# Kernel optimization log

Measured on AMD Instinct MI355X. Metric: run time of the kernel, lower is better.

## Reference

```python
import jax, jax.numpy as jnp
import numpy as np

N = 25000      # nodes
E = 400000     # edges (before self-loops)
F_IN = 128     # num_node_features
HID = 16       # hidden_channels
HEADS = 12     # GAT heads
OUT = 32       # output_channels


def setup_inputs() -> dict:
    key = jax.random.key(0)
    ks = jax.random.split(key, 16)
    def glorot(k, shape):
        fan_in = shape[0]
        return jax.random.normal(k, shape, jnp.float32) / np.sqrt(fan_in)
    return {
        "x": jax.random.normal(ks[0], (N, 1, F_IN), jnp.float32),
        "edge_index": jax.random.randint(ks[1], (2, E), 0, N, jnp.int64),
        # GCNConv 1
        "W1": glorot(ks[2], (F_IN, HID)),
        "b1": jnp.zeros((HID,), jnp.float32),
        # GATConv (heads=12, concat)
        "Wg": glorot(ks[3], (HID, HEADS * HID)),
        "att_src": jax.random.normal(ks[4], (HEADS, HID), jnp.float32) * 0.1,
        "att_dst": jax.random.normal(ks[5], (HEADS, HID), jnp.float32) * 0.1,
        "bg": jnp.zeros((HEADS * HID,), jnp.float32),
        # GCNConv 2 and 3
        "W2": glorot(ks[6], (HEADS * HID, HID)),
        "b2": jnp.zeros((HID,), jnp.float32),
        "W3": glorot(ks[7], (HID, HID)),
        "b3": jnp.zeros((HID,), jnp.float32),
        # final Linear
        "Wlin": glorot(ks[8], (HID, OUT)),
        "blin": jnp.zeros((OUT,), jnp.float32),
    }


def _add_self_loops(edge_index, n):
    loop = jnp.arange(n, dtype=edge_index.dtype)
    src = jnp.concatenate([edge_index[0], loop])
    dst = jnp.concatenate([edge_index[1], loop])
    return src, dst


def _gcn_conv(x, W, b, src, dst, n):
    # PyG GCNConv: symmetric normalization with self-loops (already in src/dst)
    h = x @ W                                            # [N, C]
    deg = jax.ops.segment_sum(jnp.ones_like(dst, jnp.float32), dst, n)
    dinv = jnp.where(deg > 0, jax.lax.rsqrt(deg), 0.0)   # deg^-0.5
    norm = dinv[src] * dinv[dst]                         # [E']
    out = jax.ops.segment_sum(h[src] * norm[:, None], dst, n)
    return out + b


def _gat_conv(x, Wg, att_src, att_dst, bg, src, dst, n):
    # PyG GATConv, concat=True, negative_slope=0.2, self-loops in src/dst
    h = (x @ Wg).reshape(n, HEADS, HID)                  # [N, H, C]
    a_s = jnp.sum(h * att_src, axis=-1)                  # [N, H]
    a_d = jnp.sum(h * att_dst, axis=-1)                  # [N, H]
    e = a_s[src] + a_d[dst]                              # [E', H]
    e = jnp.where(e > 0, e, 0.2 * e)                     # leaky_relu
    m = jax.ops.segment_max(e, dst, n)                   # stable softmax per dst
    ex = jnp.exp(e - m[dst])
    denom = jax.ops.segment_sum(ex, dst, n)
    alpha = ex / denom[dst]                              # [E', H]
    out = jax.ops.segment_sum(alpha[:, :, None] * h[src], dst, n)  # [N, H, C]
    return out.reshape(n, HEADS * HID) + bg


def reference(x, edge_index, W1, b1, Wg, att_src, att_dst, bg, W2, b2, W3, b3, Wlin, blin):
    n = x.shape[0]
    src, dst = _add_self_loops(edge_index, n)
    xs = x.squeeze(1)                                    # [N, F]
    x1 = jax.nn.relu(_gcn_conv(xs, W1, b1, src, dst, n))
    # dropout p=0.5 is identity in eval mode
    x2 = jax.nn.elu(_gat_conv(x1, Wg, att_src, att_dst, bg, src, dst, n))
    x3 = jax.nn.relu(_gcn_conv(x2, W2, b2, src, dst, n))
    x4 = jax.nn.relu(_gcn_conv(x3, W3, b3, src, dst, n)) + x3
    x4 = jnp.mean(x4, axis=0, keepdims=True)             # [1, HID]
    return x4 @ Wlin + blin                              # [1, OUT]
```

## Files before the change

kernel.cpp:

```cpp
#include <hip/hip_runtime.h>

#define F_IN 128
#define HID 16
#define HEADS 12
#define HF (HEADS*HID)
#define OUT_C 32

__global__ void k_detect(const int* __restrict__ ei, int E, int* __restrict__ flag) {
    int t = threadIdx.x;
    long long half = (long long)E;
    int acc = 0;
    #pragma unroll
    for (int i = 0; i < 8; i++) {
        long long k = ((long long)(t + i * 256) * half) / 2048;
        acc |= ei[2 * k + 1];
    }
    if (acc) atomicOr(&flag[1], 1);
}

__global__ void k_convert(const void* __restrict__ ei, int E, const int* __restrict__ flag,
                          int* __restrict__ src32, int* __restrict__ dst32,
                          int* __restrict__ count) {
    int e = blockIdx.x * blockDim.x + threadIdx.x;
    if (e >= E) return;
    int s, d;
    if (flag[1] == 0) {
        const long long* p = (const long long*)ei;
        s = (int)p[e];
        d = (int)p[(size_t)E + e];
    } else {
        const int* p = (const int*)ei;
        s = p[e];
        d = p[(size_t)E + e];
    }
    src32[e] = s;
    dst32[e] = d;
    atomicAdd(&count[d], 1);
}


__global__ void k_scan(const int* __restrict__ count, int* __restrict__ rowstart,
                       float* __restrict__ dinv, int n) {
    __shared__ int part[1024];
    int t = threadIdx.x;
    int chunk = (n + 1023) >> 10;
    int beg = t * chunk;
    int end = beg + chunk; if (end > n) end = n;
    int s = 0;
    for (int i = beg; i < end; i++) s += count[i];
    part[t] = s;
    __syncthreads();
    for (int off = 1; off < 1024; off <<= 1) {
        int v = (t >= off) ? part[t - off] : 0;
        __syncthreads();
        part[t] += v;
        __syncthreads();
    }
    int run = (t == 0) ? 0 : part[t - 1];
    for (int i = beg; i < end; i++) {
        rowstart[i] = run;
        int c = count[i];
        run += c;
        dinv[i] = rsqrtf((float)(c + 1));
    }
    if (t == 1023) rowstart[n] = run;
}

__global__ void k_fill(const int* __restrict__ srcA, const int* __restrict__ dstA, int E,
                       const int* __restrict__ rowstart, int* __restrict__ cursor,
                       int* __restrict__ csr) {
    int e = blockIdx.x * blockDim.x + threadIdx.x;
    if (e < E) {
        int d = dstA[e];
        int p = atomicAdd(&cursor[d], 1);
        csr[rowstart[d] + p] = srcA[e];
    }
}


__global__ void k_gemm1(const float* __restrict__ x, const float* __restrict__ W,
                        float* __restrict__ h, int n) {
    __shared__ float sW[F_IN * HID];
    __shared__ float sX[16][F_IN + 1];
    int t = threadIdx.x;
    for (int i = t; i < F_IN * HID; i += 256) sW[i] = W[i];
    int node0 = blockIdx.x * 16;
    for (int i = t; i < 16 * F_IN; i += 256) {
        int r = i >> 7, c = i & 127;
        int node = node0 + r;
        sX[r][c] = (node < n) ? x[node * F_IN + c] : 0.f;
    }
    __syncthreads();
    int ln = t >> 4, c = t & 15;
    float acc = 0.f;
    #pragma unroll 8
    for (int k = 0; k < F_IN; k++) acc += sX[ln][k] * sW[k * HID + c];
    int node = node0 + ln;
    if (node < n) h[node * HID + c] = acc;
}

__global__ void k_gemm_gat(const float* __restrict__ x1, const float* __restrict__ Wg,
                           const float* __restrict__ att_s, const float* __restrict__ att_d,
                           float* __restrict__ hg, float* __restrict__ a_s,
                           float* __restrict__ a_d, int n) {
    int c = threadIdx.x;
    int lane = c & 63;
    int hh = c >> 4, ci = c & 15;
    float ats = att_s[c];
    float atd = att_d[c];
    float wcol[HID];
    #pragma unroll
    for (int k = 0; k < HID; k++) wcol[k] = Wg[k * HF + c];
    for (int node = blockIdx.x; node < n; node += gridDim.x) {
        float xv = x1[node * HID + (lane & 15)];
        float acc = 0.f;
        #pragma unroll
        for (int k = 0; k < HID; k++) acc += __shfl(xv, k) * wcol[k];
        hg[(size_t)node * HF + c] = acc;
        float vs = acc * ats, vd = acc * atd;
        #pragma unroll
        for (int msk = 8; msk >= 1; msk >>= 1) {
            vs += __shfl_xor(vs, msk);
            vd += __shfl_xor(vd, msk);
        }
        if (ci == 0) {
            a_s[node * HEADS + hh] = vs;
            a_d[node * HEADS + hh] = vd;
        }
    }
}

__global__ void k_gemm2(const float* __restrict__ x2, const float* __restrict__ W,
                        float* __restrict__ h, int n) {
    __shared__ float sW[HF * HID];
    __shared__ float sX[16][HF + 1];
    int t = threadIdx.x;
    for (int i = t; i < HF * HID; i += 256) sW[i] = W[i];
    int node0 = blockIdx.x * 16;
    for (int i = t; i < 16 * HF; i += 256) {
        int r = i / HF, c = i % HF;
        int node = node0 + r;
        sX[r][c] = (node < n) ? x2[(size_t)node * HF + c] : 0.f;
    }
    __syncthreads();
    int ln = t >> 4, c = t & 15;
    float acc = 0.f;
    #pragma unroll 8
    for (int k = 0; k < HF; k++) acc += sX[ln][k] * sW[k * HID + c];
    int node = node0 + ln;
    if (node < n) h[node * HID + c] = acc;
}

__global__ void k_gemm3(const float* __restrict__ x3, const float* __restrict__ W,
                        float* __restrict__ h, int n) {
    __shared__ float sW[HID * HID];
    __shared__ float sX[16][HID + 1];
    int t = threadIdx.x;
    sW[t] = W[t];
    int node0 = blockIdx.x * 16;
    int r = t >> 4, cc = t & 15;
    int nd = node0 + r;
    sX[r][cc] = (nd < n) ? x3[nd * HID + cc] : 0.f;
    __syncthreads();
    float acc = 0.f;
    #pragma unroll
    for (int k = 0; k < HID; k++) acc += sX[r][k] * sW[k * HID + cc];
    if (nd < n) h[nd * HID + cc] = acc;
}


__global__ void k_gcn_agg(const float* __restrict__ h, const int* __restrict__ rowstart,
                          const int* __restrict__ csr, const float* __restrict__ dinv,
                          const float* __restrict__ bias, const float* __restrict__ resid,
                          float* __restrict__ out, int n) {
    int node = (blockIdx.x * blockDim.x + threadIdx.x) >> 6;
    int lane = threadIdx.x & 63;
    if (node >= n) return;
    int c = lane & 15, jj = lane >> 4;
    float dn = dinv[node];
    int base = rowstart[node], deg = rowstart[node + 1] - base;
    float acc = (jj == 0) ? h[node * HID + c] * dn : 0.f;
    for (int j = jj; j < deg; j += 4) {
        int s = csr[base + j];
        acc += h[s * HID + c] * dinv[s];
    }
    acc += __shfl_xor(acc, 16);
    acc += __shfl_xor(acc, 32);
    if (lane < 16) {
        float v = fmaxf(acc * dn + bias[c], 0.f);
        if (resid) v += resid[node * HID + c];
        out[node * HID + c] = v;
    }
}

__global__ void k_gat_agg(const float* __restrict__ hg, const float* __restrict__ a_s,
                          const float* __restrict__ a_d, const int* __restrict__ rowstart,
                          const int* __restrict__ csr, const float* __restrict__ bg,
                          float* __restrict__ x2, int n) {
    int node = (blockIdx.x * blockDim.x + threadIdx.x) >> 6;
    int lane = threadIdx.x & 63;
    if (node >= n) return;
    int base = rowstart[node], deg = rowstart[node + 1] - base;

    float mh[3], sh[3], acc[3], adh[3];
    int hhv[3];
    #pragma unroll
    for (int it = 0; it < 3; it++) {
        int c = lane + 64 * it;
        int hh = c >> 4;
        hhv[it] = hh;
        float ad = a_d[node * HEADS + hh];
        adh[it] = ad;
        float e = a_s[node * HEADS + hh] + ad;
        e = (e > 0.f) ? e : 0.2f * e;
        mh[it] = e;
        sh[it] = 1.f;
        acc[it] = hg[(size_t)node * HF + c];
    }

    int j = 0;
    for (; j + 2 <= deg; j += 2) {
        int src0 = csr[base + j], src1 = csr[base + j + 1];
        float as0[3], as1[3], hg0[3], hg1[3];
        #pragma unroll
        for (int it = 0; it < 3; it++) {
            as0[it] = a_s[src0 * HEADS + hhv[it]];
            as1[it] = a_s[src1 * HEADS + hhv[it]];
            hg0[it] = hg[(size_t)src0 * HF + lane + 64 * it];
            hg1[it] = hg[(size_t)src1 * HF + lane + 64 * it];
        }
        #pragma unroll
        for (int it = 0; it < 3; it++) {
            float e = as0[it] + adh[it];
            e = (e > 0.f) ? e : 0.2f * e;
            float d = e - mh[it];
            float p = __expf(d);
            if (d > 8.f) {
                float rp = __expf(-d);
                acc[it] = acc[it] * rp + hg0[it];
                sh[it]  = sh[it] * rp + 1.f;
                mh[it] = e;
            } else {
                acc[it] += p * hg0[it];
                sh[it]  += p;
            }
            e = as1[it] + adh[it];
            e = (e > 0.f) ? e : 0.2f * e;
            d = e - mh[it];
            p = __expf(d);
            if (d > 8.f) {
                float rp = __expf(-d);
                acc[it] = acc[it] * rp + hg1[it];
                sh[it]  = sh[it] * rp + 1.f;
                mh[it] = e;
            } else {
                acc[it] += p * hg1[it];
                sh[it]  += p;
            }
        }
    }
    if (j < deg) {
        int src0 = csr[base + j];
        #pragma unroll
        for (int it = 0; it < 3; it++) {
            float hgv = hg[(size_t)src0 * HF + lane + 64 * it];
            float e = a_s[src0 * HEADS + hhv[it]] + adh[it];
            e = (e > 0.f) ? e : 0.2f * e;
            float d = e - mh[it];
            float p = __expf(d);
            if (d > 8.f) {
                float rp = __expf(-d);
                acc[it] = acc[it] * rp + hgv;
                sh[it]  = sh[it] * rp + 1.f;
                mh[it] = e;
            } else {
                acc[it] += p * hgv;
                sh[it]  += p;
            }
        }
    }

    #pragma unroll
    for (int it = 0; it < 3; it++) {
        int c = lane + 64 * it;
        float v = acc[it] / sh[it] + bg[c];
        v = (v > 0.f) ? v : (__expf(v) - 1.f);
        x2[(size_t)node * HF + c] = v;
    }
}


__global__ void k_mean(const float* __restrict__ x4, float* __restrict__ red, int n) {
    __shared__ float sd[16][17];
    int t = threadIdx.x;
    int ln = t >> 4, c = t & 15;
    float acc = 0.f;
    for (int node = blockIdx.x * 16 + ln; node < n; node += gridDim.x * 16)
        acc += x4[node * HID + c];
    sd[ln][c] = acc;
    __syncthreads();
    for (int off = 8; off >= 1; off >>= 1) {
        if (ln < off) sd[ln][c] += sd[ln + off][c];
        __syncthreads();
    }
    if (ln == 0) atomicAdd(&red[c], sd[0][c]);
}

__global__ void k_final(const float* __restrict__ red, const float* __restrict__ Wlin,
                        const float* __restrict__ blin, float* __restrict__ out, float invN) {
    int o = threadIdx.x;
    if (o >= OUT_C) return;
    float acc = blin[o];
    #pragma unroll
    for (int c = 0; c < HID; c++) acc += (red[c] * invN) * Wlin[c * OUT_C + o];
    out[o] = acc;
}


extern "C" void kernel_launch(void* const* d_in, const int* in_sizes, int n_in,
                              void* d_out, int out_size, void* d_ws, size_t ws_size,
                              hipStream_t stream) {
    const float* x     = (const float*)d_in[0];
    const void*  ei    = d_in[1];
    const float* W1    = (const float*)d_in[2];
    const float* b1    = (const float*)d_in[3];
    const float* Wg    = (const float*)d_in[4];
    const float* att_s = (const float*)d_in[5];
    const float* att_d = (const float*)d_in[6];
    const float* bg    = (const float*)d_in[7];
    const float* W2    = (const float*)d_in[8];
    const float* b2    = (const float*)d_in[9];
    const float* W3    = (const float*)d_in[10];
    const float* b3    = (const float*)d_in[11];
    const float* Wlin  = (const float*)d_in[12];
    const float* blin  = (const float*)d_in[13];
    float* out = (float*)d_out;

    int N = in_sizes[0] / F_IN;
    int E = in_sizes[1] / 2;

    char* w = (char*)d_ws;
    size_t off = 0;
    auto alloc = [&](size_t bytes) -> void* {
        void* p = w + off;
        off += (bytes + 255) & ~(size_t)255;
        return p;
    };
    int*   flag     = (int*)alloc(256);
    int*   src32    = (int*)alloc((size_t)E * 4);
    int*   dst32    = (int*)alloc((size_t)E * 4);
    int*   count    = (int*)alloc((size_t)N * 4);
    int*   rowstart = (int*)alloc((size_t)(N + 1) * 4);
    int*   cursor   = (int*)alloc((size_t)N * 4);
    int*   csr      = (int*)alloc((size_t)E * 4);
    float* dinv     = (float*)alloc((size_t)N * 4);
    float* h1       = (float*)alloc((size_t)N * HID * 4);
    float* x1       = (float*)alloc((size_t)N * HID * 4);
    float* hg       = (float*)alloc((size_t)N * HF * 4);
    float* a_s      = (float*)alloc((size_t)N * HEADS * 4);
    float* a_d      = (float*)alloc((size_t)N * HEADS * 4);
    float* x2       = (float*)alloc((size_t)N * HF * 4);
    float* h2       = (float*)alloc((size_t)N * HID * 4);
    float* x3       = (float*)alloc((size_t)N * HID * 4);
    float* h3       = (float*)alloc((size_t)N * HID * 4);
    float* x4       = (float*)alloc((size_t)N * HID * 4);
    float* red      = (float*)alloc(64);
    if (off > ws_size) return;

    hipMemsetAsync(flag, 0, 256, stream);
    hipMemsetAsync(count, 0, (size_t)N * 4, stream);
    hipMemsetAsync(cursor, 0, (size_t)N * 4, stream);
    hipMemsetAsync(red, 0, 64, stream);

    int eb = (E + 255) / 256;
    int nb16 = (N + 15) / 16;
    int nbw  = (N + 3) / 4;

    k_detect<<<1, 256, 0, stream>>>((const int*)ei, E, flag);
    k_convert<<<eb, 256, 0, stream>>>(ei, E, flag, src32, dst32, count);
    k_scan<<<1, 1024, 0, stream>>>(count, rowstart, dinv, N);
    k_fill<<<eb, 256, 0, stream>>>(src32, dst32, E, rowstart, cursor, csr);

    k_gemm1<<<nb16, 256, 0, stream>>>(x, W1, h1, N);
    k_gcn_agg<<<nbw, 256, 0, stream>>>(h1, rowstart, csr, dinv, b1, nullptr, x1, N);

    k_gemm_gat<<<2048, 192, 0, stream>>>(x1, Wg, att_s, att_d, hg, a_s, a_d, N);
    k_gat_agg<<<nbw, 256, 0, stream>>>(hg, a_s, a_d, rowstart, csr, bg, x2, N);

    k_gemm2<<<nb16, 256, 0, stream>>>(x2, W2, h2, N);
    k_gcn_agg<<<nbw, 256, 0, stream>>>(h2, rowstart, csr, dinv, b2, nullptr, x3, N);

    k_gemm3<<<nb16, 256, 0, stream>>>(x3, W3, h3, N);
    k_gcn_agg<<<nbw, 256, 0, stream>>>(h3, rowstart, csr, dinv, b3, x3, x4, N);

    k_mean<<<128, 256, 0, stream>>>(x4, red, N);
    k_final<<<1, 64, 0, stream>>>(red, Wlin, blin, out, 1.0f / (float)N);
}
```

Measured before the change: 351.2 us.

## Merge memsets, shuffle-based GAT softmax per head, unroll GCN gather

```diff
diff --git a/kernel.cpp b/kernel.cpp
--- a/kernel.cpp
+++ b/kernel.cpp
@@ -7,6 +7,7 @@
 #define OUT_C 32
 
 __global__ void k_detect(const int* __restrict__ ei, int E, int* __restrict__ flag) {
+    __shared__ int sacc[256];
     int t = threadIdx.x;
     long long half = (long long)E;
     int acc = 0;
@@ -15,7 +16,13 @@
         long long k = ((long long)(t + i * 256) * half) / 2048;
         acc |= ei[2 * k + 1];
     }
-    if (acc) atomicOr(&flag[1], 1);
+    sacc[t] = acc;
+    __syncthreads();
+    for (int off = 128; off >= 1; off >>= 1) {
+        if (t < off) sacc[t] |= sacc[t + off];
+        __syncthreads();
+    }
+    if (t == 0) flag[1] = sacc[0];
 }
 
 __global__ void k_convert(const void* __restrict__ ei, int E, const int* __restrict__ flag,
@@ -180,9 +187,16 @@
     float dn = dinv[node];
     int base = rowstart[node], deg = rowstart[node + 1] - base;
     float acc = (jj == 0) ? h[node * HID + c] * dn : 0.f;
-    for (int j = jj; j < deg; j += 4) {
-        int s = csr[base + j];
-        acc += h[s * HID + c] * dinv[s];
+    int j = jj;
+    for (; j + 4 < deg; j += 8) {
+        int s0 = csr[base + j], s1 = csr[base + j + 4];
+        float d0 = dinv[s0], d1 = dinv[s1];
+        float h0 = h[s0 * HID + c], h1 = h[s1 * HID + c];
+        acc += h0 * d0 + h1 * d1;
+    }
+    if (j < deg) {
+        int s0 = csr[base + j];
+        acc += h[s0 * HID + c] * dinv[s0];
     }
     acc += __shfl_xor(acc, 16);
     acc += __shfl_xor(acc, 32);
@@ -202,91 +216,77 @@
     if (node >= n) return;
     int base = rowstart[node], deg = rowstart[node + 1] - base;
 
-    float mh[3], sh[3], acc[3], adh[3];
-    int hhv[3];
-    #pragma unroll
-    for (int it = 0; it < 3; it++) {
-        int c = lane + 64 * it;
-        int hh = c >> 4;
-        hhv[it] = hh;
-        float ad = a_d[node * HEADS + hh];
-        adh[it] = ad;
-        float e = a_s[node * HEADS + hh] + ad;
-        e = (e > 0.f) ? e : 0.2f * e;
-        mh[it] = e;
-        sh[it] = 1.f;
-        acc[it] = hg[(size_t)node * HF + c];
+    int hA = lane % 12;
+    int hh0 = lane >> 4;
+    int hh1 = (lane + 64) >> 4;
+    int hh2 = (lane + 128) >> 4;
+
+    float adA = a_d[node * HEADS + hA];
+    float e0 = a_s[node * HEADS + hA] + adA;
+    e0 = (e0 > 0.f) ? e0 : 0.2f * e0;
+    float m = e0, s = 1.f;
+    float acc0 = hg[(size_t)node * HF + lane];
+    float acc1 = hg[(size_t)node * HF + lane + 64];
+    float acc2 = hg[(size_t)node * HF + lane + 128];
+
+#define GAT_EDGE(AS, G0, G1, G2)                                      \
+    {                                                                 \
+        float e = (AS) + adA;                                         \
+        e = (e > 0.f) ? e : 0.2f * e;                                 \
+        float d = e - m;                                              \
+        float p = __expf(d);                                          \
+        if (__any(d > 8.f)) {                       \
+            bool big = d > 8.f;                                       \
+            float rp = big ? __expf(-d) : 1.f;                        \
+            float pe = big ? 1.f : p;                                 \
+            s = s * rp + pe;                                          \
+            if (big) m = e;                                           \
+            acc0 = acc0 * __shfl(rp, hh0) + __shfl(pe, hh0) * (G0);   \
+            acc1 = acc1 * __shfl(rp, hh1) + __shfl(pe, hh1) * (G1);   \
+            acc2 = acc2 * __shfl(rp, hh2) + __shfl(pe, hh2) * (G2);   \
+        } else {                                                      \
+            s += p;                                                   \
+            acc0 += __shfl(p, hh0) * (G0);                            \
+            acc1 += __shfl(p, hh1) * (G1);                            \
+            acc2 += __shfl(p, hh2) * (G2);                            \
+        }                                                             \
     }
 
     int j = 0;
     for (; j + 2 <= deg; j += 2) {
-        int src0 = csr[base + j], src1 = csr[base + j + 1];
-        float as0[3], as1[3], hg0[3], hg1[3];
-        #pragma unroll
-        for (int it = 0; it < 3; it++) {
-            as0[it] = a_s[src0 * HEADS + hhv[it]];
-            as1[it] = a_s[src1 * HEADS + hhv[it]];
-            hg0[it] = hg[(size_t)src0 * HF + lane + 64 * it];
-            hg1[it] = hg[(size_t)src1 * HF + lane + 64 * it];
-        }
-        #pragma unroll
-        for (int it = 0; it < 3; it++) {
-            float e = as0[it] + adh[it];
-            e = (e > 0.f) ? e : 0.2f * e;
-            float d = e - mh[it];
-            float p = __expf(d);
-            if (d > 8.f) {
-                float rp = __expf(-d);
-                acc[it] = acc[it] * rp + hg0[it];
-                sh[it]  = sh[it] * rp + 1.f;
-                mh[it] = e;
-            } else {
-                acc[it] += p * hg0[it];
-                sh[it]  += p;
-            }
-            e = as1[it] + adh[it];
-            e = (e > 0.f) ? e : 0.2f * e;
-            d = e - mh[it];
-            p = __expf(d);
-            if (d > 8.f) {
-                float rp = __expf(-d);
-                acc[it] = acc[it] * rp + hg1[it];
-                sh[it]  = sh[it] * rp + 1.f;
-                mh[it] = e;
-            } else {
-                acc[it] += p * hg1[it];
-                sh[it]  += p;
-            }
-        }
+        int s0 = csr[base + j], s1 = csr[base + j + 1];
+        float as0 = a_s[s0 * HEADS + hA];
+        float as1 = a_s[s1 * HEADS + hA];
+        float g00 = hg[(size_t)s0 * HF + lane];
+        float g01 = hg[(size_t)s0 * HF + lane + 64];
+        float g02 = hg[(size_t)s0 * HF + lane + 128];
+        float g10 = hg[(size_t)s1 * HF + lane];
+        float g11 = hg[(size_t)s1 * HF + lane + 64];
+        float g12 = hg[(size_t)s1 * HF + lane + 128];
+        GAT_EDGE(as0, g00, g01, g02)
+        GAT_EDGE(as1, g10, g11, g12)
     }
     if (j < deg) {
-        int src0 = csr[base + j];
-        #pragma unroll
-        for (int it = 0; it < 3; it++) {
-            float hgv = hg[(size_t)src0 * HF + lane + 64 * it];
-            float e = a_s[src0 * HEADS + hhv[it]] + adh[it];
-            e = (e > 0.f) ? e : 0.2f * e;
-            float d = e - mh[it];
-            float p = __expf(d);
-            if (d > 8.f) {
-                float rp = __expf(-d);
-                acc[it] = acc[it] * rp + hgv;
-                sh[it]  = sh[it] * rp + 1.f;
-                mh[it] = e;
-            } else {
-                acc[it] += p * hgv;
-                sh[it]  += p;
-            }
-        }
-    }
-
-    #pragma unroll
-    for (int it = 0; it < 3; it++) {
-        int c = lane + 64 * it;
-        float v = acc[it] / sh[it] + bg[c];
-        v = (v > 0.f) ? v : (__expf(v) - 1.f);
-        x2[(size_t)node * HF + c] = v;
-    }
+        int s0 = csr[base + j];
+        float as0 = a_s[s0 * HEADS + hA];
+        float g00 = hg[(size_t)s0 * HF + lane];
+        float g01 = hg[(size_t)s0 * HF + lane + 64];
+        float g02 = hg[(size_t)s0 * HF + lane + 128];
+        GAT_EDGE(as0, g00, g01, g02)
+    }
+#undef GAT_EDGE
+
+    float is = 1.f / s;
+    float i0 = __shfl(is, hh0), i1 = __shfl(is, hh1), i2 = __shfl(is, hh2);
+    float v0 = acc0 * i0 + bg[lane];
+    float v1 = acc1 * i1 + bg[lane + 64];
+    float v2 = acc2 * i2 + bg[lane + 128];
+    v0 = (v0 > 0.f) ? v0 : (__expf(v0) - 1.f);
+    v1 = (v1 > 0.f) ? v1 : (__expf(v1) - 1.f);
+    v2 = (v2 > 0.f) ? v2 : (__expf(v2) - 1.f);
+    x2[(size_t)node * HF + lane]       = v0;
+    x2[(size_t)node * HF + lane + 64]  = v1;
+    x2[(size_t)node * HF + lane + 128] = v2;
 }
 
 
@@ -347,11 +347,13 @@
         return p;
     };
     int*   flag     = (int*)alloc(256);
+    int*   count    = (int*)alloc((size_t)N * 4);
+    int*   cursor   = (int*)alloc((size_t)N * 4);
+    float* red      = (float*)alloc(64);
+    size_t zbytes   = (size_t)((char*)red + 256 - (char*)count);
     int*   src32    = (int*)alloc((size_t)E * 4);
     int*   dst32    = (int*)alloc((size_t)E * 4);
-    int*   count    = (int*)alloc((size_t)N * 4);
     int*   rowstart = (int*)alloc((size_t)(N + 1) * 4);
-    int*   cursor   = (int*)alloc((size_t)N * 4);
     int*   csr      = (int*)alloc((size_t)E * 4);
     float* dinv     = (float*)alloc((size_t)N * 4);
     float* h1       = (float*)alloc((size_t)N * HID * 4);
@@ -364,13 +366,9 @@
     float* x3       = (float*)alloc((size_t)N * HID * 4);
     float* h3       = (float*)alloc((size_t)N * HID * 4);
     float* x4       = (float*)alloc((size_t)N * HID * 4);
-    float* red      = (float*)alloc(64);
     if (off > ws_size) return;
 
-    hipMemsetAsync(flag, 0, 256, stream);
-    hipMemsetAsync(count, 0, (size_t)N * 4, stream);
-    hipMemsetAsync(cursor, 0, (size_t)N * 4, stream);
-    hipMemsetAsync(red, 0, 64, stream);
+    hipMemsetAsync(count, 0, zbytes, stream);
 
     int eb = (E + 255) / 256;
     int nb16 = (N + 15) / 16;
```

Measured after the change: 336.1 us. 1.04x faster.
